# Kernel tuning notes

Measured on AMD Instinct MI355X. Metric: run time of the kernel, lower is better.

## Reference

```python
import jax, jax.numpy as jnp
import numpy as np

B, T, D, H, O = 64, 512, 256, 1024, 1


def setup_inputs() -> dict:
    key = jax.random.key(0)
    ks = jax.random.split(key, 11)
    s_in = 1.0 / np.sqrt(H)
    def u(k, shape):
        return jax.random.uniform(k, shape, jnp.float32, -s_in, s_in)
    return {
        "x": jax.random.normal(ks[0], (B, T, D), jnp.float32),
        "w_ih_0": u(ks[1], (4 * H, D)),
        "w_hh_0": u(ks[2], (4 * H, H)),
        "b_ih_0": u(ks[3], (4 * H,)),
        "b_hh_0": u(ks[4], (4 * H,)),
        "w_ih_1": u(ks[5], (4 * H, H)),
        "w_hh_1": u(ks[6], (4 * H, H)),
        "b_ih_1": u(ks[7], (4 * H,)),
        "b_hh_1": u(ks[8], (4 * H,)),
        "w_lin": u(ks[9], (O, H)),
        "b_lin": u(ks[10], (O,)),
    }


def _lstm_layer(x, w_ih, w_hh, b_ih, b_hh):
    # x: [B, T, Din] -> h_seq: [B, T, H]. PyTorch gate order: i, f, g, o.
    # Precompute input projections for all timesteps (one big GEMM).
    xp = jnp.einsum("btd,gd->tbg", x, w_ih) + b_ih + b_hh  # [T, B, 4H]
    h0 = jnp.zeros((x.shape[0], w_hh.shape[1]), x.dtype)
    c0 = jnp.zeros_like(h0)

    def step(carry, xp_t):
        h, c = carry
        gates = xp_t + h @ w_hh.T  # [B, 4H]
        i, f, g, o = jnp.split(gates, 4, axis=-1)
        i = jax.nn.sigmoid(i)
        f = jax.nn.sigmoid(f)
        g = jnp.tanh(g)
        o = jax.nn.sigmoid(o)
        c = f * c + i * g
        h = o * jnp.tanh(c)
        return (h, c), h

    (_, _), h_seq = jax.lax.scan(step, (h0, c0), xp)  # h_seq: [T, B, H]
    return jnp.transpose(h_seq, (1, 0, 2))  # [B, T, H]


def reference(x, w_ih_0, w_hh_0, b_ih_0, b_hh_0,
              w_ih_1, w_hh_1, b_ih_1, b_hh_1, w_lin, b_lin):
    h1 = _lstm_layer(x, w_ih_0, w_hh_0, b_ih_0, b_hh_0)
    h2 = _lstm_layer(h1, w_ih_1, w_hh_1, b_ih_1, b_hh_1)
    return h2[:, -1, :] @ w_lin.T + b_lin  # [B, O]
```

## Files before the change

### kernel.cpp

```cpp
#include <hip/hip_runtime.h>


#define T_STEPS 512
#define NWG 256
#define LDS_W     131072
#define LDS_GBUF  (64 * 33 * 4)
#define LDS_CBUF  (64 * 9 * 4)
#define LDS_OFFS  (32 * 4)
#define LDS_PEX   16384
#define SMEM_BYTES (LDS_W + LDS_GBUF + LDS_CBUF + LDS_OFFS + LDS_PEX)

typedef int v4i  __attribute__((ext_vector_type(4)));
typedef int v16i __attribute__((ext_vector_type(16)));

__device__ __forceinline__ v16i zero16() {
    v16i z;
#pragma unroll
    for (int i = 0; i < 16; ++i) z[i] = 0;
    return z;
}

__device__ __forceinline__ void load_f16_nw(const char* b0p, v4i* o) {
    const char* b1p = b0p + 4096;
    const char* b2p = b0p + 8192;
    const char* b3p = b0p + 12288;
    asm volatile(
        "global_load_dwordx4 %0, %16, off sc0 sc1\n\t"
        "global_load_dwordx4 %1, %16, off offset:16 sc0 sc1\n\t"
        "global_load_dwordx4 %2, %16, off offset:2048 sc0 sc1\n\t"
        "global_load_dwordx4 %3, %16, off offset:2064 sc0 sc1\n\t"
        "global_load_dwordx4 %4, %17, off sc0 sc1\n\t"
        "global_load_dwordx4 %5, %17, off offset:16 sc0 sc1\n\t"
        "global_load_dwordx4 %6, %17, off offset:2048 sc0 sc1\n\t"
        "global_load_dwordx4 %7, %17, off offset:2064 sc0 sc1\n\t"
        "global_load_dwordx4 %8, %18, off sc0 sc1\n\t"
        "global_load_dwordx4 %9, %18, off offset:16 sc0 sc1\n\t"
        "global_load_dwordx4 %10, %18, off offset:2048 sc0 sc1\n\t"
        "global_load_dwordx4 %11, %18, off offset:2064 sc0 sc1\n\t"
        "global_load_dwordx4 %12, %19, off sc0 sc1\n\t"
        "global_load_dwordx4 %13, %19, off offset:16 sc0 sc1\n\t"
        "global_load_dwordx4 %14, %19, off offset:2048 sc0 sc1\n\t"
        "global_load_dwordx4 %15, %19, off offset:2064 sc0 sc1"
        : "=&v"(o[0]), "=&v"(o[1]), "=&v"(o[2]), "=&v"(o[3]),
          "=&v"(o[4]), "=&v"(o[5]), "=&v"(o[6]), "=&v"(o[7]),
          "=&v"(o[8]), "=&v"(o[9]), "=&v"(o[10]), "=&v"(o[11]),
          "=&v"(o[12]), "=&v"(o[13]), "=&v"(o[14]), "=&v"(o[15])
        : "v"(b0p), "v"(b1p), "v"(b2p), "v"(b3p)
        : "memory");
}

#define WAIT_BIND(cntstr, b)                                                   \
    asm volatile("s_waitcnt vmcnt(" cntstr ")"                                 \
        : "+v"((b)[0]), "+v"((b)[1]), "+v"((b)[2]), "+v"((b)[3]),              \
          "+v"((b)[4]), "+v"((b)[5]), "+v"((b)[6]), "+v"((b)[7]),              \
          "+v"((b)[8]), "+v"((b)[9]), "+v"((b)[10]), "+v"((b)[11]),            \
          "+v"((b)[12]), "+v"((b)[13]), "+v"((b)[14]), "+v"((b)[15])           \
        :: "memory")

__device__ __forceinline__ void st16_wt(void* p, v4i v) {
    asm volatile("global_store_dwordx4 %0, %1, off sc0 sc1" :: "v"(p), "v"(v) : "memory");
}
__device__ __forceinline__ void store_slot(unsigned* p, unsigned v) {
    asm volatile("global_store_dword %0, %1, off sc0 sc1" :: "v"(p), "v"(v) : "memory");
}
__device__ __forceinline__ v4i ld4_mall(const unsigned* p) {
    v4i r;
    asm volatile("global_load_dwordx4 %0, %1, off sc0 sc1\n\ts_waitcnt vmcnt(0)"
                 : "=v"(r) : "v"(p) : "memory");
    return r;
}
__device__ __forceinline__ void waitcnt0() {
    asm volatile("s_waitcnt vmcnt(0)" ::: "memory");
}
__device__ __forceinline__ bool slots_ok(v4i v, unsigned thr) {
    return ((unsigned)v.x >= thr) & ((unsigned)v.y >= thr) &
           ((unsigned)v.z >= thr) & ((unsigned)v.w >= thr);
}

__device__ __forceinline__ void split_a(v4i A0, v4i A1, v4i& HI, v4i& LO) {
    HI.x = (int)__builtin_amdgcn_perm((unsigned)A0.y, (unsigned)A0.x, 0x07050301u);
    HI.y = (int)__builtin_amdgcn_perm((unsigned)A0.w, (unsigned)A0.z, 0x07050301u);
    HI.z = (int)__builtin_amdgcn_perm((unsigned)A1.y, (unsigned)A1.x, 0x07050301u);
    HI.w = (int)__builtin_amdgcn_perm((unsigned)A1.w, (unsigned)A1.z, 0x07050301u);
    LO.x = (int)(__builtin_amdgcn_perm((unsigned)A0.y, (unsigned)A0.x, 0x06040200u) ^ 0x80808080u);
    LO.y = (int)(__builtin_amdgcn_perm((unsigned)A0.w, (unsigned)A0.z, 0x06040200u) ^ 0x80808080u);
    LO.z = (int)(__builtin_amdgcn_perm((unsigned)A1.y, (unsigned)A1.x, 0x06040200u) ^ 0x80808080u);
    LO.w = (int)(__builtin_amdgcn_perm((unsigned)A1.w, (unsigned)A1.z, 0x06040200u) ^ 0x80808080u);
}

__device__ __forceinline__ void consume8(const v4i* hb, const char* wbase,
                                         v16i& ahh, v16i& amid)
{
#pragma unroll
    for (int s = 0; s < 8; ++s) {
        v4i HI, LO; split_a(hb[2 * s], hb[2 * s + 1], HI, LO);
        v4i BH = *(const v4i*)(wbase + s * 2048);
        v4i BL = *(const v4i*)(wbase + s * 2048 + 1024);
        ahh  = __builtin_amdgcn_mfma_i32_32x32x32_i8(HI, BH, ahh, 0, 0, 0);
        amid = __builtin_amdgcn_mfma_i32_32x32x32_i8(HI, BL, amid, 0, 0, 0);
        amid = __builtin_amdgcn_mfma_i32_32x32x32_i8(LO, BH, amid, 0, 0, 0);
    }
}

__device__ __forceinline__ void kstep(const short* __restrict__ ap,
                                      const char* __restrict__ wl,
                                      v16i& ahh, v16i& amid)
{
    v4i A0 = *(const v4i*)ap;
    v4i A1 = *(const v4i*)(ap + 8);
    v4i HI, LO; split_a(A0, A1, HI, LO);
    v4i BH = *(const v4i*)wl;
    v4i BL = *(const v4i*)(wl + 1024);
    ahh  = __builtin_amdgcn_mfma_i32_32x32x32_i8(HI, BH, ahh, 0, 0, 0);
    amid = __builtin_amdgcn_mfma_i32_32x32x32_i8(HI, BL, amid, 0, 0, 0);
    amid = __builtin_amdgcn_mfma_i32_32x32x32_i8(LO, BH, amid, 0, 0, 0);
}

__global__ void quant_x(const float* __restrict__ x, short* __restrict__ xq, int n)
{
    int i = blockIdx.x * 256 + threadIdx.x;
    if (i < n) {
        float v = x[i] * 2048.f;
        v = fminf(fmaxf(v, -32767.f), 32767.f);
        xq[i] = (short)__float2int_rn(v);
    }
}

__global__ void quant_w(const float* __restrict__ wih0, const float* __restrict__ whh0,
                        const float* __restrict__ wih1, const float* __restrict__ whh1,
                        char* __restrict__ wimg)
{
    int gid = blockIdx.x * 256 + threadIdx.x;
    if (gid >= 256 * 64 * 64) return;
    int lane = gid & 63;
    int s    = (gid >> 6) & 63;
    int wg   = gid >> 12;
    int layer = wg >> 7, nblk = wg & 127;
    int col = nblk * 32 + (lane & 31);
    int ro  = (col & 3) * 1024 + (col >> 2);
    int k0  = s * 32 + (lane >> 5) * 16;
    char* dst = wimg + (size_t)wg * LDS_W + s * 2048 + lane * 16;
#pragma unroll
    for (int j = 0; j < 16; ++j) {
        int k = k0 + j;
        float w = 0.f;
        if (layer == 0) {
            if (k < 256)       w = wih0[ro * 256 + k];
            else if (k < 1280) w = whh0[ro * 1024 + (k - 256)];
        } else {
            if (k < 1024)      w = wih1[ro * 1024 + k];
            else               w = whh1[ro * 1024 + (k - 1024)];
        }
        int q  = __float2int_rn(w * 524288.f);
        int hi = (q + 128) >> 8;
        int lo = q - (hi << 8);
        dst[j]        = (char)hi;
        dst[1024 + j] = (char)lo;
    }
}

__global__ void __launch_bounds__(256, 1) lstm_main(
    const short* __restrict__ xq, const char* __restrict__ wimg,
    const float* __restrict__ bih0, const float* __restrict__ bhh0,
    const float* __restrict__ bih1, const float* __restrict__ bhh1,
    short* __restrict__ h0q, short* __restrict__ h2q,
    float* __restrict__ h2f, unsigned* gslots)
{
    extern __shared__ char smem[];
    char*  wlds = smem;
    float* gbuf = (float*)(smem + LDS_W);
    float* cbuf = (float*)(smem + LDS_W + LDS_GBUF);
    float* offs = (float*)(smem + LDS_W + LDS_GBUF + LDS_CBUF);
    int*   pexch = (int*)(smem + LDS_W + LDS_GBUF + LDS_CBUF + LDS_OFFS);

    const int wg    = blockIdx.x;
    const int layer = wg >> 7;
    const int nblk  = wg & 127;
    const int tid   = threadIdx.x;
    const int lane  = tid & 63;
    const int w     = tid >> 6;
    const int RB    = w >> 1;
    const int kh    = w & 1;
    const float inv33 = 1.1641532182693481e-10f;

    {
        const v4i* src = (const v4i*)(wimg + (size_t)wg * LDS_W);
        v4i* dst = (v4i*)wlds;
        for (int i = tid; i < LDS_W / 16; i += 256) dst[i] = src[i];
    }
    for (int i = tid; i < 64 * 9; i += 256) cbuf[i] = 0.f;
    __syncthreads();

    if (tid < 32) {
        const int c  = tid;
        const int ns = (layer == 0) ? 40 : 64;
        int cs_x = 0, cs_h = 0;
        for (int s = 0; s < ns; ++s) {
            int sum = 0;
#pragma unroll
            for (int half = 0; half < 2; ++half) {
                const signed char* ph = (const signed char*)(wlds + s * 2048 + (half * 32 + c) * 16);
#pragma unroll
                for (int j = 0; j < 16; ++j)
                    sum += 256 * (int)ph[j] + (int)ph[1024 + j];
            }
            if (layer == 0 && s < 8) cs_x += sum; else cs_h += sum;
        }
        const int col = nblk * 32 + c;
        const int ro  = (col & 3) * 1024 + (col >> 2);
        const float bias = (layer == 0) ? (bih0[ro] + bhh0[ro]) : (bih1[ro] + bhh1[ro]);
        float off = 128.f * (float)cs_h * inv33 + bias;
        if (layer == 0) off += 128.f * (float)cs_x * 9.313225746154785e-10f;
        offs[c] = off;
    }
    __syncthreads();

    const int mrow = RB * 32 + (lane & 31);
    const int ksub = (lane >> 5) * 16;
    const int j0   = nblk * 8;
    const int sj   = j0 >> 5;
    const int hbj  = (j0 >> 4) & 1;
    const int inj  = (j0 & 15) * 2;

    for (int p = 0; p <= T_STEPS + 1; ++p) {
        const bool actL0 = (layer == 0) && (p < T_STEPS);
        const bool actL1 = (layer == 1) && (p >= 2);
        const bool active = actL0 || actL1;

        v16i ahh = zero16(), amid = zero16();

        if (layer == 0) {
            v16i ax = zero16(), mx = zero16();
            if (actL0 && kh == 0) {
                const short* axp = xq + ((size_t)mrow * 512 + p) * 256 + ksub;
#pragma unroll
                for (int s = 0; s < 8; ++s)
                    kstep(axp + s * 32, wlds + s * 2048 + lane * 16, ax, mx);
            }
            if (p > 0) {
                if (tid < 64) {
                    const unsigned thr = (tid < 32) ? (unsigned)p
                                                    : (unsigned)(p > 5 ? p - 5 : 0);
                    const unsigned* sp = gslots + tid * 4;
                    for (;;) {
                        v4i v = ld4_mall(sp);
                        if (!__ballot(!slots_ok(v, thr))) break;
                        __builtin_amdgcn_s_sleep(3);
                    }
                }
                __syncthreads();
                asm volatile("" ::: "memory");
            }
            if (actL0 && p > 0) {
                const char* f0 = (const char*)h0q + ((p - 1) & 7) * 131072
                               + RB * 65536 + lane * 32 + kh * 32768;
                const char* W = wlds + lane * 16 + (8 + kh * 16) * 2048;
                v4i b0[16], b1[16];
                waitcnt0();
                load_f16_nw(f0, b0);
                load_f16_nw(f0 + 16384, b1);
                WAIT_BIND("16", b0); consume8(b0, W, ahh, amid);
                WAIT_BIND("0", b1);  consume8(b1, W + 8 * 2048, ahh, amid);
            }
            if (actL0 && kh == 0) {
#pragma unroll
                for (int r = 0; r < 16; ++r) {
                    ahh[r]  += 8 * ax[r];
                    amid[r] += 8 * mx[r];
                }
            }
        } else {
            if (actL1) {
                if (tid < 32) {
                    const unsigned thr = (unsigned)(p - 1);
                    const unsigned* sp = gslots + tid * 4;
                    for (;;) {
                        v4i v = ld4_mall(sp);
                        if (!__ballot(!slots_ok(v, thr))) break;
                        __builtin_amdgcn_s_sleep(3);
                    }
                }
                __syncthreads();
                asm volatile("" ::: "memory");
                const char* f0 = (const char*)h0q + ((p - 2) & 7) * 131072
                               + RB * 65536 + lane * 32 + kh * 32768;
                const char* W = wlds + lane * 16 + kh * 16 * 2048;
                v4i b0[16], b1[16];
                waitcnt0();
                load_f16_nw(f0, b0);
                load_f16_nw(f0 + 16384, b1);
                WAIT_BIND("16", b0); consume8(b0, W, ahh, amid);
                WAIT_BIND("0", b1);  consume8(b1, W + 8 * 2048, ahh, amid);
            }
            if (p > 0) {
                if (tid < 64) {
                    const unsigned* sp = gslots + 128 + (tid & 31) * 4;
                    const unsigned thr = (unsigned)p;
                    for (;;) {
                        v4i v = ld4_mall(sp);
                        if (!__ballot(!slots_ok(v, thr))) break;
                        __builtin_amdgcn_s_sleep(3);
                    }
                }
                __syncthreads();
                asm volatile("" ::: "memory");
            }
            if (actL1 && p > 2) {
                const char* f2 = (const char*)h2q + ((p - 3) & 3) * 131072
                               + RB * 65536 + lane * 32 + kh * 32768;
                const char* W = wlds + lane * 16 + (32 + kh * 16) * 2048;
                v4i b0[16], b1[16];
                waitcnt0();
                load_f16_nw(f2, b0);
                load_f16_nw(f2 + 16384, b1);
                WAIT_BIND("16", b0); consume8(b0, W, ahh, amid);
                WAIT_BIND("0", b1);  consume8(b1, W + 8 * 2048, ahh, amid);
            }
        }

        if (active && kh == 1) {
            int* pxm = pexch + RB * 2048;
#pragma unroll
            for (int i = 0; i < 16; ++i) pxm[i * 64 + lane] = ahh[i];
#pragma unroll
            for (int i = 0; i < 16; ++i) pxm[(16 + i) * 64 + lane] = amid[i];
        }
        __syncthreads();
        if (active && kh == 0) {
            const int* pxm = pexch + RB * 2048;
            const int rbase = RB * 32 + 4 * (lane >> 5);
            const int c = lane & 31;
#pragma unroll
            for (int r = 0; r < 16; ++r) {
                int th = ahh[r]  + pxm[r * 64 + lane];
                int tm = amid[r] + pxm[(16 + r) * 64 + lane];
                float g = ((float)th * 65536.f + (float)tm * 256.f) * inv33
                        + offs[c];
                int row = rbase + (r & 3) + 8 * (r >> 2);
                gbuf[row * 33 + c] = g;
            }
        }
        __syncthreads();
        if (active && tid < 64) {
            const int r = tid;
            unsigned hq[8];
            float hf[8];
#pragma unroll
            for (int u = 0; u < 8; ++u) {
                const float gi = gbuf[r * 33 + 4 * u + 0];
                const float gf = gbuf[r * 33 + 4 * u + 1];
                const float gg = gbuf[r * 33 + 4 * u + 2];
                const float go = gbuf[r * 33 + 4 * u + 3];
                const float i_ = 1.f / (1.f + __expf(-gi));
                const float f_ = 1.f / (1.f + __expf(-gf));
                const float g_ = 1.f - 2.f / (__expf(2.f * gg) + 1.f);
                const float o_ = 1.f / (1.f + __expf(-go));
                float c_ = f_ * cbuf[r * 9 + u] + i_ * g_;
                cbuf[r * 9 + u] = c_;
                const float h_ = o_ * (1.f - 2.f / (__expf(2.f * c_) + 1.f));
                hq[u] = (unsigned)(unsigned short)(short)__float2int_rn(h_ * 16384.f);
                hf[u] = h_;
            }
            v4i pk;
            pk.x = (int)(hq[0] | (hq[1] << 16));
            pk.y = (int)(hq[2] | (hq[3] << 16));
            pk.z = (int)(hq[4] | (hq[5] << 16));
            pk.w = (int)(hq[6] | (hq[7] << 16));
            char* hw = (layer == 0)
                     ? (char*)h0q + (p & 7) * 131072
                     : (char*)h2q + ((p - 2) & 3) * 131072;
            hw += (r >> 5) * 65536 + sj * 2048 + ((r & 31) + 32 * hbj) * 32 + inj;
            st16_wt(hw, pk);
            if (layer == 1 && p == T_STEPS + 1) {
#pragma unroll
                for (int u = 0; u < 8; ++u) h2f[r * 1024 + j0 + u] = hf[u];
            }
        }
        if (p < T_STEPS + 1) {
            waitcnt0();
            __syncthreads();
            if (tid == 0)
                store_slot(gslots + wg, (unsigned)(p + 1));
        }
    }
}

__global__ void final_lin(const float* __restrict__ h2f, const float* __restrict__ wlin,
                          const float* __restrict__ blin, float* __restrict__ out)
{
    const int b = blockIdx.x;
    const int l = threadIdx.x;
    float s = 0.f;
    for (int j = l; j < 1024; j += 64) s += h2f[b * 1024 + j] * wlin[j];
#pragma unroll
    for (int off = 32; off; off >>= 1) s += __shfl_down(s, off);
    if (l == 0) out[b] = s + blin[0];
}

extern "C" void kernel_launch(void* const* d_in, const int* in_sizes, int n_in,
                              void* d_out, int out_size, void* d_ws, size_t ws_size,
                              hipStream_t stream)
{
    const float* x    = (const float*)d_in[0];
    const float* wih0 = (const float*)d_in[1];
    const float* whh0 = (const float*)d_in[2];
    const float* bih0 = (const float*)d_in[3];
    const float* bhh0 = (const float*)d_in[4];
    const float* wih1 = (const float*)d_in[5];
    const float* whh1 = (const float*)d_in[6];
    const float* bih1 = (const float*)d_in[7];
    const float* bhh1 = (const float*)d_in[8];
    const float* wlin = (const float*)d_in[9];
    const float* blin = (const float*)d_in[10];

    char* ws = (char*)d_ws;
    unsigned* gslots = (unsigned*)ws;
    short* h0q = (short*)(ws + 65536);
    short* h2q = (short*)(ws + 65536 + 1048576);
    float* h2f = (float*)(ws + 65536 + 1572864);
    short* xq  = (short*)(ws + 65536 + 1835008);
    char*  wimg = ws + 65536 + 1835008 + 16777216;

    hipMemsetAsync(ws, 0, 65536, stream);

    quant_x<<<32768, 256, 0, stream>>>(x, xq, 64 * 512 * 256);
    quant_w<<<4096, 256, 0, stream>>>(wih0, whh0, wih1, whh1, wimg);

    hipFuncSetAttribute((const void*)lstm_main,
        hipFuncAttributeMaxDynamicSharedMemorySize, SMEM_BYTES);

    lstm_main<<<NWG, 256, SMEM_BYTES, stream>>>(xq, wimg, bih0, bhh0, bih1, bhh1,
                                                h0q, h2q, h2f, gslots);
    final_lin<<<64, 64, 0, stream>>>(h2f, wlin, blin, (float*)d_out);
}
```

Before: 4.394 ms.

## Split layer-1 waves by input stream so h1 and h2 products overlap

In layer-1 workgroups, the four waves are now split by input stream instead of by K-half. Two waves wait for and consume the full layer-0 hidden state (h0q), and the other two wait for and consume the recurrent layer-1 state (h2q), each over the whole K range with double-buffered loads. This removes the two block-wide barriers between the h0 and h2 phases, so the two dependency waits and their dot products can proceed at the same time. In exchange, each wave performs twice the K-loop work and the partial-sum exchange is remapped per layer.

Result: slower. 5.356 ms (+21.9%).

```diff
diff --git a/kernel.cpp b/kernel.cpp
--- a/kernel.cpp
+++ b/kernel.cpp
@@ -181,6 +181,8 @@
     const int w     = tid >> 6;
     const int RB    = w >> 1;
     const int kh    = w & 1;
+    const int rb1   = w & 1;
+    const int str   = w >> 1;
     const float inv33 = 1.1641532182693481e-10f;
 
     {
@@ -270,74 +272,83 @@
                 }
             }
         } else {
-            if (actL1) {
-                if (tid < 32) {
-                    const unsigned thr = (unsigned)(p - 1);
-                    const unsigned* sp = gslots + tid * 4;
+            if (str == 0) {
+                if (actL1) {
+                    const unsigned thr = (lane < 32) ? (unsigned)(p - 1) : 0u;
+                    const unsigned* sp = gslots + (lane & 31) * 4;
                     for (;;) {
                         v4i v = ld4_mall(sp);
                         if (!__ballot(!slots_ok(v, thr))) break;
                         __builtin_amdgcn_s_sleep(3);
                     }
-                }
-                __syncthreads();
-                asm volatile("" ::: "memory");
-                const char* f0 = (const char*)h0q + ((p - 2) & 7) * 131072
-                               + RB * 65536 + lane * 32 + kh * 32768;
-                const char* W = wlds + lane * 16 + kh * 16 * 2048;
-                v4i b0[16], b1[16];
-                waitcnt0();
-                load_f16_nw(f0, b0);
-                load_f16_nw(f0 + 16384, b1);
-                WAIT_BIND("16", b0); consume8(b0, W, ahh, amid);
-                WAIT_BIND("0", b1);  consume8(b1, W + 8 * 2048, ahh, amid);
-            }
-            if (p > 0) {
-                if (tid < 64) {
-                    const unsigned* sp = gslots + 128 + (tid & 31) * 4;
+                    asm volatile("" ::: "memory");
+                    const char* f0 = (const char*)h0q + ((p - 2) & 7) * 131072
+                                   + rb1 * 65536 + lane * 32;
+                    const char* W = wlds + lane * 16;
+                    v4i b0[16], b1[16];
+                    waitcnt0();
+                    load_f16_nw(f0, b0);
+                    load_f16_nw(f0 + 16384, b1);
+                    WAIT_BIND("16", b0); consume8(b0, W, ahh, amid);
+                    load_f16_nw(f0 + 32768, b0);
+                    WAIT_BIND("16", b1); consume8(b1, W + 8 * 2048, ahh, amid);
+                    load_f16_nw(f0 + 49152, b1);
+                    WAIT_BIND("16", b0); consume8(b0, W + 16 * 2048, ahh, amid);
+                    WAIT_BIND("0", b1);  consume8(b1, W + 24 * 2048, ahh, amid);
+                }
+            } else {
+                if (p > 0) {
+                    const unsigned* sp = gslots + 128 + (lane & 31) * 4;
                     const unsigned thr = (unsigned)p;
                     for (;;) {
                         v4i v = ld4_mall(sp);
                         if (!__ballot(!slots_ok(v, thr))) break;
                         __builtin_amdgcn_s_sleep(3);
                     }
-                }
-                __syncthreads();
-                asm volatile("" ::: "memory");
-            }
-            if (actL1 && p > 2) {
-                const char* f2 = (const char*)h2q + ((p - 3) & 3) * 131072
-                               + RB * 65536 + lane * 32 + kh * 32768;
-                const char* W = wlds + lane * 16 + (32 + kh * 16) * 2048;
-                v4i b0[16], b1[16];
-                waitcnt0();
-                load_f16_nw(f2, b0);
-                load_f16_nw(f2 + 16384, b1);
-                WAIT_BIND("16", b0); consume8(b0, W, ahh, amid);
-                WAIT_BIND("0", b1);  consume8(b1, W + 8 * 2048, ahh, amid);
-            }
-        }
-
-        if (active && kh == 1) {
-            int* pxm = pexch + RB * 2048;
-#pragma unroll
-            for (int i = 0; i < 16; ++i) pxm[i * 64 + lane] = ahh[i];
-#pragma unroll
-            for (int i = 0; i < 16; ++i) pxm[(16 + i) * 64 + lane] = amid[i];
-        }
-        __syncthreads();
-        if (active && kh == 0) {
-            const int* pxm = pexch + RB * 2048;
-            const int rbase = RB * 32 + 4 * (lane >> 5);
-            const int c = lane & 31;
-#pragma unroll
-            for (int r = 0; r < 16; ++r) {
-                int th = ahh[r]  + pxm[r * 64 + lane];
-                int tm = amid[r] + pxm[(16 + r) * 64 + lane];
-                float g = ((float)th * 65536.f + (float)tm * 256.f) * inv33
-                        + offs[c];
-                int row = rbase + (r & 3) + 8 * (r >> 2);
-                gbuf[row * 33 + c] = g;
+                    asm volatile("" ::: "memory");
+                }
+                if (actL1 && p > 2) {
+                    const char* f2 = (const char*)h2q + ((p - 3) & 3) * 131072
+                                   + rb1 * 65536 + lane * 32;
+                    const char* W = wlds + lane * 16 + 32 * 2048;
+                    v4i b0[16], b1[16];
+                    waitcnt0();
+                    load_f16_nw(f2, b0);
+                    load_f16_nw(f2 + 16384, b1);
+                    WAIT_BIND("16", b0); consume8(b0, W, ahh, amid);
+                    load_f16_nw(f2 + 32768, b0);
+                    WAIT_BIND("16", b1); consume8(b1, W + 8 * 2048, ahh, amid);
+                    load_f16_nw(f2 + 49152, b1);
+                    WAIT_BIND("16", b0); consume8(b0, W + 16 * 2048, ahh, amid);
+                    WAIT_BIND("0", b1);  consume8(b1, W + 24 * 2048, ahh, amid);
+                }
+            }
+        }
+
+        {
+            const int  rbIdx = (layer == 0) ? RB : rb1;
+            const bool isPub = (layer == 0) ? (kh == 1) : (str == 1);
+            if (active && isPub) {
+                int* pxm = pexch + rbIdx * 2048;
+#pragma unroll
+                for (int i = 0; i < 16; ++i) pxm[i * 64 + lane] = ahh[i];
+#pragma unroll
+                for (int i = 0; i < 16; ++i) pxm[(16 + i) * 64 + lane] = amid[i];
+            }
+            __syncthreads();
+            if (active && !isPub) {
+                const int* pxm = pexch + rbIdx * 2048;
+                const int rbase = rbIdx * 32 + 4 * (lane >> 5);
+                const int c = lane & 31;
+#pragma unroll
+                for (int r = 0; r < 16; ++r) {
+                    int th = ahh[r]  + pxm[r * 64 + lane];
+                    int tm = amid[r] + pxm[(16 + r) * 64 + lane];
+                    float g = ((float)th * 65536.f + (float)tm * 256.f) * inv33
+                            + offs[c];
+                    int row = rbase + (r & 3) + 8 * (r >> 2);
+                    gbuf[row * 33 + c] = g;
+                }
             }
         }
         __syncthreads();
```
